# Optimization experiments

Hardware: AMD Instinct MI355X
Metric: run time of the kernel (lower is better)

## Reference

```python
import jax, jax.numpy as jnp
import numpy as np

B, T, C, H = 4096, 96, 256, 64  # batch, seq (<= BLOCK_SIZE=96), N_EMBED, head_size


def setup_inputs() -> dict:
    key = jax.random.key(0)
    k1, k2, k3, k4 = jax.random.split(key, 4)
    x = jax.random.normal(k1, (B, T, C), dtype=jnp.float32)
    # nn.Linear(C, H, bias=False) stores W as [H, C]; we keep [C, H] so y = x @ W.
    scale = 1.0 / jnp.sqrt(C)
    Wk = jax.random.normal(k2, (C, H), dtype=jnp.float32) * scale
    Wq = jax.random.normal(k3, (C, H), dtype=jnp.float32) * scale
    Wv = jax.random.normal(k4, (C, H), dtype=jnp.float32) * scale
    return {"x": x, "Wk": Wk, "Wq": Wq, "Wv": Wv}


def reference(x, Wk, Wq, Wv):
    Bx, Tx, Cx = x.shape
    k = x @ Wk                      # [B, T, H]
    q = x @ Wq                      # [B, T, H]
    v = x @ Wv                      # [B, T, H]
    # NOTE: original scales by C**-0.5 (embed dim), not head_size**-0.5.
    wei = jnp.einsum('bth,bsh->bts', q, k) * (Cx ** -0.5)  # [B, T, T]
    causal = jnp.tril(jnp.ones((Tx, Tx), dtype=bool))
    wei = jnp.where(causal, wei, -jnp.inf)
    wei = jax.nn.softmax(wei, axis=-1)
    # dropout is identity at eval time
    return jnp.einsum('bts,bsh->bth', wei, v)  # [B, T, H]
```

## Files before the change

kernel.cpp:

```cpp
#include <hip/hip_runtime.h>
#include <cstddef>


typedef __bf16 bf16x8 __attribute__((ext_vector_type(8)));
typedef float f32x4 __attribute__((ext_vector_type(4)));

#define GLOAD_LDS16(gp, lp)                                                     \
  __builtin_amdgcn_global_load_lds(                                             \
      (const __attribute__((address_space(1))) void*)(gp),                      \
      (__attribute__((address_space(3))) void*)(lp), 16, 0, 0)

static __device__ __forceinline__ unsigned short f2bf_u16(float f) {
  union { float f; unsigned int u; } c; c.f = f;
  return (unsigned short)((c.u + 0x7FFFu + ((c.u >> 16) & 1u)) >> 16);
}

__global__ void pack_w(const float* __restrict__ Wk, const float* __restrict__ Wq,
                       const float* __restrict__ Wv, unsigned short* __restrict__ pack) {
  int idx = blockIdx.x * blockDim.x + threadIdx.x;
  if (idx >= 6144) return;
  int lane = idx & 63;
  int t = idx >> 6;
  int nt = t & 3;
  int p  = (t >> 2) % 3;
  int kt = t / 12;
  const float* W = (p == 0) ? Wk : (p == 1) ? Wq : Wv;
  int k0 = kt * 32 + (lane >> 4) * 8;
  int n  = nt * 16 + (lane & 15);
  unsigned short* dst = pack + (size_t)idx * 8;
#pragma unroll
  for (int j = 0; j < 8; ++j) dst[j] = f2bf_u16(W[(size_t)(k0 + j) * 64 + n]);
}

#define LDK 72
#define LDP 104
#define LDV 104

__global__ __launch_bounds__(768, 6) void head_fused(
    const float* __restrict__ x, const unsigned short* __restrict__ pack,
    float* __restrict__ out) {
  __shared__ __attribute__((aligned(16))) unsigned char smem[68352];
  unsigned short* SA  = (unsigned short*)smem;
  unsigned short* ks2 = (unsigned short*)(smem + 39936);
  float*          rsm = (float*)(smem + 67584);

  const int w    = threadIdx.x >> 6;
  const int half = w >= 6;
  const int w6   = w - 6 * half;
  const int lane = threadIdx.x & 63;
  const int lo   = lane & 15;
  const int hi   = lane >> 4;

  const int bb = 2 * blockIdx.x + half;
  const float* __restrict__ xb = x + (size_t)bb * (96 * 256);

  unsigned short* SAh  = SA  + half * (96 * LDP);
  unsigned short* ks2h = ks2 + half * (96 * LDK);
  float*          rsh  = rsm + half * 96;

  f32x4 acc[3][4];
#pragma unroll
  for (int p = 0; p < 3; ++p)
#pragma unroll
    for (int nt = 0; nt < 4; ++nt) acc[p][nt] = (f32x4){0.f, 0.f, 0.f, 0.f};

  const int am = 16 * w6 + lo;
  const float* xrow = xb + (size_t)am * 256 + hi * 8;

  GLOAD_LDS16((const char*)pack + (size_t)threadIdx.x * 16,
              smem + (size_t)w * 1024);
  f32x4 a0 = *(const f32x4*)(xrow);
  f32x4 a1 = *(const f32x4*)(xrow + 4);
  __syncthreads();

  for (int kt = 0; kt < 8; ++kt) {
    const int cur = kt & 1;
    f32x4 na0, na1;
    if (kt < 7) {
      GLOAD_LDS16((const char*)pack + (size_t)(kt + 1) * 12288 + (size_t)threadIdx.x * 16,
                  smem + (size_t)(1 - cur) * 12288 + (size_t)w * 1024);
      na0 = *(const f32x4*)(xrow + (kt + 1) * 32);
      na1 = *(const f32x4*)(xrow + (kt + 1) * 32 + 4);
    }
    union { bf16x8 v; unsigned short u[8]; } af;
#pragma unroll
    for (int j = 0; j < 4; ++j) { af.u[j] = f2bf_u16(a0[j]); af.u[4 + j] = f2bf_u16(a1[j]); }
    const unsigned short* pb = (const unsigned short*)(smem + cur * 12288);
#pragma unroll
    for (int p = 0; p < 3; ++p) {
#pragma unroll
      for (int nt = 0; nt < 4; ++nt) {
        bf16x8 bf = *(const bf16x8*)(pb + ((p * 4 + nt) * 64 + lane) * 8);
        acc[p][nt] = __builtin_amdgcn_mfma_f32_16x16x32_bf16(af.v, bf, acc[p][nt], 0, 0, 0);
      }
    }
    if (kt < 7) { a0 = na0; a1 = na1; }
    __syncthreads();
  }

  unsigned short vv[16];
#pragma unroll
  for (int nt = 0; nt < 4; ++nt) {
#pragma unroll
    for (int r = 0; r < 4; ++r) {
      int row = 16 * w6 + hi * 4 + r;
      int col = 16 * nt + lo;
      ks2h[row * LDK + col] = f2bf_u16(acc[0][nt][r]);
      SAh [row * LDP + col] = f2bf_u16(acc[1][nt][r]);
      vv[nt * 4 + r] = f2bf_u16(acc[2][nt][r]);
    }
  }
  __syncthreads();

  f32x4 sacc[6];
#pragma unroll
  for (int jt = 0; jt < 6; ++jt) sacc[jt] = (f32x4){0.f, 0.f, 0.f, 0.f};

  bf16x8 qf0 = *(const bf16x8*)(SAh + (16 * w6 + lo) * LDP + hi * 8);
  bf16x8 qf1 = *(const bf16x8*)(SAh + (16 * w6 + lo) * LDP + 32 + hi * 8);
  for (int jt = 0; jt <= w6; ++jt) {
    bf16x8 kf0 = *(const bf16x8*)(ks2h + (16 * jt + lo) * LDK + hi * 8);
    bf16x8 kf1 = *(const bf16x8*)(ks2h + (16 * jt + lo) * LDK + 32 + hi * 8);
    sacc[jt] = __builtin_amdgcn_mfma_f32_16x16x32_bf16(qf0, kf0, sacc[jt], 0, 0, 0);
    sacc[jt] = __builtin_amdgcn_mfma_f32_16x16x32_bf16(qf1, kf1, sacc[jt], 0, 0, 0);
  }

#pragma unroll
  for (int r = 0; r < 4; ++r) {
    int row = 16 * w6 + hi * 4 + r;
    float pr[6];
    float mx = -1e30f;
    for (int jt = 0; jt <= w6; ++jt) {
      int col = 16 * jt + lo;
      float s = sacc[jt][r] * 0.0625f;
      s = (col <= row) ? s : -1e30f;
      pr[jt] = s;
      mx = fmaxf(mx, s);
    }
#pragma unroll
    for (int off = 1; off < 16; off <<= 1) mx = fmaxf(mx, __shfl_xor(mx, off, 64));
    float sum = 0.f;
    for (int jt = 0; jt <= w6; ++jt) {
      float p = __expf(pr[jt] - mx);
      pr[jt] = p;
      sum += p;
    }
#pragma unroll
    for (int off = 1; off < 16; off <<= 1) sum += __shfl_xor(sum, off, 64);
#pragma unroll
    for (int jt = 0; jt < 6; ++jt) {
      float p = (jt <= w6) ? pr[jt] : 0.f;
      SAh[row * LDP + 16 * jt + lo] = f2bf_u16(p);
    }
    if (lo == 0) rsh[row] = sum;
  }
  __syncthreads();

  unsigned short* vT = ks2h;
#pragma unroll
  for (int nt = 0; nt < 4; ++nt) {
#pragma unroll
    for (int r = 0; r < 4; ++r) {
      int row = 16 * w6 + hi * 4 + r;
      int col = 16 * nt + lo;
      vT[col * LDV + row] = vv[nt * 4 + r];
    }
  }
  __syncthreads();

  f32x4 oacc[4];
#pragma unroll
  for (int nt = 0; nt < 4; ++nt) oacc[nt] = (f32x4){0.f, 0.f, 0.f, 0.f};

  const int ksmax = (16 * w6 + 15) >> 5;
  for (int ks = 0; ks <= ksmax; ++ks) {
    bf16x8 pf = *(const bf16x8*)(SAh + (16 * w6 + lo) * LDP + ks * 32 + hi * 8);
#pragma unroll
    for (int nt = 0; nt < 4; ++nt) {
      bf16x8 vf = *(const bf16x8*)(vT + (16 * nt + lo) * LDV + ks * 32 + hi * 8);
      oacc[nt] = __builtin_amdgcn_mfma_f32_16x16x32_bf16(pf, vf, oacc[nt], 0, 0, 0);
    }
  }

  float* __restrict__ ob = out + (size_t)bb * (96 * 64);
#pragma unroll
  for (int r = 0; r < 4; ++r) {
    int row = 16 * w6 + hi * 4 + r;
    float inv = 1.0f / rsh[row];
#pragma unroll
    for (int nt = 0; nt < 4; ++nt) {
      ob[row * 64 + 16 * nt + lo] = oacc[nt][r] * inv;
    }
  }
}

extern "C" void kernel_launch(void* const* d_in, const int* in_sizes, int n_in,
                              void* d_out, int out_size, void* d_ws, size_t ws_size,
                              hipStream_t stream) {
  const float* x  = (const float*)d_in[0];
  const float* Wk = (const float*)d_in[1];
  const float* Wq = (const float*)d_in[2];
  const float* Wv = (const float*)d_in[3];
  float* out = (float*)d_out;
  unsigned short* pack = (unsigned short*)d_ws;

  const int B = in_sizes[0] / (96 * 256);

  pack_w<<<24, 256, 0, stream>>>(Wk, Wq, Wv, pack);
  head_fused<<<B / 2, 768, 0, stream>>>(x, pack, out);
}
```

Before: 662.1 us.

## Deepen QKV projection pipeline and stage output through LDS for coalesced stores

The QKV projection loop is restructured to process two k-tiles per barrier. Packed weights for two k-steps are loaded into double-buffered 24 KB LDS regions, and x rows are prefetched two iterations ahead in registers. Explicit s_waitcnt vmcnt and raw s_barrier calls replace __syncthreads. The aim is to keep more global loads in flight and halve the number of barriers in the memory-latency-bound projection. The epilogue now writes normalized outputs to LDS and stores them back as 16-byte vectors, which makes the global writes coalesced. The cost is extra register pressure and one more block-wide barrier.

```diff
diff --git a/kernel.cpp b/kernel.cpp
--- a/kernel.cpp
+++ b/kernel.cpp
@@ -9,6 +9,10 @@
   __builtin_amdgcn_global_load_lds(                                             \
       (const __attribute__((address_space(1))) void*)(gp),                      \
       (__attribute__((address_space(3))) void*)(lp), 16, 0, 0)
+
+#define FENCE() asm volatile("" ::: "memory")
+#define WAITVM(N) asm volatile("s_waitcnt vmcnt(" #N ")" ::: "memory")
+#define BAR() do { __builtin_amdgcn_s_barrier(); FENCE(); } while (0)
 
 static __device__ __forceinline__ unsigned short f2bf_u16(float f) {
   union { float f; unsigned int u; } c; c.f = f;
@@ -67,34 +71,86 @@
   const int am = 16 * w6 + lo;
   const float* xrow = xb + (size_t)am * 256 + hi * 8;
 
-  GLOAD_LDS16((const char*)pack + (size_t)threadIdx.x * 16,
-              smem + (size_t)w * 1024);
-  f32x4 a0 = *(const f32x4*)(xrow);
-  f32x4 a1 = *(const f32x4*)(xrow + 4);
-  __syncthreads();
-
-  for (int kt = 0; kt < 8; ++kt) {
-    const int cur = kt & 1;
-    f32x4 na0, na1;
-    if (kt < 7) {
-      GLOAD_LDS16((const char*)pack + (size_t)(kt + 1) * 12288 + (size_t)threadIdx.x * 16,
-                  smem + (size_t)(1 - cur) * 12288 + (size_t)w * 1024);
-      na0 = *(const f32x4*)(xrow + (kt + 1) * 32);
-      na1 = *(const f32x4*)(xrow + (kt + 1) * 32 + 4);
-    }
-    union { bf16x8 v; unsigned short u[8]; } af;
-#pragma unroll
-    for (int j = 0; j < 4; ++j) { af.u[j] = f2bf_u16(a0[j]); af.u[4 + j] = f2bf_u16(a1[j]); }
-    const unsigned short* pb = (const unsigned short*)(smem + cur * 12288);
-#pragma unroll
-    for (int p = 0; p < 3; ++p) {
+  f32x4 A0[4], A1[4];
+
+#define XLOAD(SL, IT) do {                         \
+    const float* xp_ = xrow + (IT) * 64;           \
+    SL[0] = *(const f32x4*)(xp_);                  \
+    SL[1] = *(const f32x4*)(xp_ + 4);              \
+    SL[2] = *(const f32x4*)(xp_ + 32);             \
+    SL[3] = *(const f32x4*)(xp_ + 36);             \
+  } while (0)
+
+#define STAGE(IT, BUFOFS) do {                                                        \
+    const char* g_ = (const char*)pack + (size_t)(2 * (IT)) * 12288                   \
+                     + (size_t)threadIdx.x * 16;                                      \
+    GLOAD_LDS16(g_,         smem + (BUFOFS) + (size_t)w * 1024);                      \
+    GLOAD_LDS16(g_ + 12288, smem + (BUFOFS) + 12288 + (size_t)w * 1024);              \
+    FENCE();                                                                          \
+  } while (0)
+
+  union bfu { bf16x8 v; unsigned short u[8]; };
+
+  auto conv = [&](const f32x4* SL, bfu& af0_, bfu& af1_) {
+#pragma unroll
+    for (int j = 0; j < 4; ++j) {
+      af0_.u[j]     = f2bf_u16(SL[0][j]);
+      af0_.u[4 + j] = f2bf_u16(SL[1][j]);
+      af1_.u[j]     = f2bf_u16(SL[2][j]);
+      af1_.u[4 + j] = f2bf_u16(SL[3][j]);
+    }
+  };
+  auto mfma24 = [&](int bufofs, bf16x8 af0_, bf16x8 af1_) {
+    const unsigned short* pb = (const unsigned short*)(smem + bufofs);
+#pragma unroll
+    for (int p = 0; p < 3; ++p)
 #pragma unroll
       for (int nt = 0; nt < 4; ++nt) {
-        bf16x8 bf = *(const bf16x8*)(pb + ((p * 4 + nt) * 64 + lane) * 8);
-        acc[p][nt] = __builtin_amdgcn_mfma_f32_16x16x32_bf16(af.v, bf, acc[p][nt], 0, 0, 0);
+        bf16x8 b0 = *(const bf16x8*)(pb + ((p * 4 + nt) * 64 + lane) * 8);
+        acc[p][nt] = __builtin_amdgcn_mfma_f32_16x16x32_bf16(af0_, b0, acc[p][nt], 0, 0, 0);
       }
-    }
-    if (kt < 7) { a0 = na0; a1 = na1; }
+    const unsigned short* pb1 = pb + 6144;
+#pragma unroll
+    for (int p = 0; p < 3; ++p)
+#pragma unroll
+      for (int nt = 0; nt < 4; ++nt) {
+        bf16x8 b1 = *(const bf16x8*)(pb1 + ((p * 4 + nt) * 64 + lane) * 8);
+        acc[p][nt] = __builtin_amdgcn_mfma_f32_16x16x32_bf16(af1_, b1, acc[p][nt], 0, 0, 0);
+      }
+  };
+
+  STAGE(0, 0);
+  XLOAD(A0, 0);
+  XLOAD(A1, 1);
+  WAITVM(8);
+  BAR();
+
+  {
+    STAGE(1, 24576);
+    bfu af0_, af1_; conv(A0, af0_, af1_);
+    XLOAD(A0, 2);
+    mfma24(0, af0_.v, af1_.v);
+    WAITVM(4);
+    BAR();
+  }
+  {
+    STAGE(2, 0);
+    bfu af0_, af1_; conv(A1, af0_, af1_);
+    XLOAD(A1, 3);
+    mfma24(24576, af0_.v, af1_.v);
+    WAITVM(4);
+    BAR();
+  }
+  {
+    STAGE(3, 24576);
+    bfu af0_, af1_; conv(A0, af0_, af1_);
+    mfma24(0, af0_.v, af1_.v);
+    WAITVM(0);
+    BAR();
+  }
+  {
+    bfu af0_, af1_; conv(A1, af0_, af1_);
+    mfma24(24576, af0_.v, af1_.v);
     __syncthreads();
   }
 
@@ -182,15 +238,20 @@
     }
   }
 
+  __syncthreads();
+  float* ot = (float*)(smem + (size_t)w * 4096);
+#pragma unroll
+  for (int r = 0; r < 4; ++r) {
+    float inv = 1.0f / rsh[16 * w6 + hi * 4 + r];
+#pragma unroll
+    for (int nt = 0; nt < 4; ++nt)
+      ot[(hi * 4 + r) * 64 + 16 * nt + lo] = oacc[nt][r] * inv;
+  }
   float* __restrict__ ob = out + (size_t)bb * (96 * 64);
 #pragma unroll
-  for (int r = 0; r < 4; ++r) {
-    int row = 16 * w6 + hi * 4 + r;
-    float inv = 1.0f / rsh[row];
-#pragma unroll
-    for (int nt = 0; nt < 4; ++nt) {
-      ob[row * 64 + 16 * nt + lo] = oacc[nt][r] * inv;
-    }
+  for (int i = 0; i < 4; ++i) {
+    f32x4 o4 = *(const f32x4*)(ot + (i * 4 + hi) * 64 + lo * 4);
+    *(f32x4*)(ob + (size_t)(16 * w6 + i * 4 + hi) * 64 + lo * 4) = o4;
   }
 }
 
```

After: 734.5 us. 1.11x slower.

## Use explicit vmcnt waits and barriers in projection loop; stage output via LDS

Applied to the files above, without the earlier changes.

The projection K-loop replaces __syncthreads with a manual s_waitcnt vmcnt(2) plus s_barrier, so the next x-row register prefetch stays in flight while the LDS weight tile is waited on. The last iteration is peeled out of the loop. The QK and softmax loops are fully unrolled over a fixed 6 tiles, with predication instead of runtime trip counts. The output is staged through per-wave LDS and written as coalesced 16-byte stores instead of scattered scalar stores. These changes add one extra barrier and depend on hand-placed waitcnt counts matching the number of outstanding loads.

```diff
diff --git a/kernel.cpp b/kernel.cpp
--- a/kernel.cpp
+++ b/kernel.cpp
@@ -9,6 +9,10 @@
   __builtin_amdgcn_global_load_lds(                                             \
       (const __attribute__((address_space(1))) void*)(gp),                      \
       (__attribute__((address_space(3))) void*)(lp), 16, 0, 0)
+
+#define FENCE() asm volatile("" ::: "memory")
+#define WAITVM(N) asm volatile("s_waitcnt vmcnt(" #N ")" ::: "memory")
+#define BAR() do { __builtin_amdgcn_s_barrier(); FENCE(); } while (0)
 
 static __device__ __forceinline__ unsigned short f2bf_u16(float f) {
   union { float f; unsigned int u; } c; c.f = f;
@@ -69,32 +73,47 @@
 
   GLOAD_LDS16((const char*)pack + (size_t)threadIdx.x * 16,
               smem + (size_t)w * 1024);
+  FENCE();
   f32x4 a0 = *(const f32x4*)(xrow);
   f32x4 a1 = *(const f32x4*)(xrow + 4);
-  __syncthreads();
-
-  for (int kt = 0; kt < 8; ++kt) {
+  WAITVM(2);
+  BAR();
+
+  for (int kt = 0; kt < 7; ++kt) {
     const int cur = kt & 1;
-    f32x4 na0, na1;
-    if (kt < 7) {
-      GLOAD_LDS16((const char*)pack + (size_t)(kt + 1) * 12288 + (size_t)threadIdx.x * 16,
-                  smem + (size_t)(1 - cur) * 12288 + (size_t)w * 1024);
-      na0 = *(const f32x4*)(xrow + (kt + 1) * 32);
-      na1 = *(const f32x4*)(xrow + (kt + 1) * 32 + 4);
-    }
+    GLOAD_LDS16((const char*)pack + (size_t)(kt + 1) * 12288 + (size_t)threadIdx.x * 16,
+                smem + (size_t)(1 - cur) * 12288 + (size_t)w * 1024);
+    FENCE();
+    f32x4 na0 = *(const f32x4*)(xrow + (kt + 1) * 32);
+    f32x4 na1 = *(const f32x4*)(xrow + (kt + 1) * 32 + 4);
+
     union { bf16x8 v; unsigned short u[8]; } af;
 #pragma unroll
     for (int j = 0; j < 4; ++j) { af.u[j] = f2bf_u16(a0[j]); af.u[4 + j] = f2bf_u16(a1[j]); }
     const unsigned short* pb = (const unsigned short*)(smem + cur * 12288);
 #pragma unroll
-    for (int p = 0; p < 3; ++p) {
+    for (int p = 0; p < 3; ++p)
 #pragma unroll
       for (int nt = 0; nt < 4; ++nt) {
         bf16x8 bf = *(const bf16x8*)(pb + ((p * 4 + nt) * 64 + lane) * 8);
         acc[p][nt] = __builtin_amdgcn_mfma_f32_16x16x32_bf16(af.v, bf, acc[p][nt], 0, 0, 0);
       }
-    }
-    if (kt < 7) { a0 = na0; a1 = na1; }
+    a0 = na0; a1 = na1;
+    WAITVM(2);
+    BAR();
+  }
+  {
+    union { bf16x8 v; unsigned short u[8]; } af;
+#pragma unroll
+    for (int j = 0; j < 4; ++j) { af.u[j] = f2bf_u16(a0[j]); af.u[4 + j] = f2bf_u16(a1[j]); }
+    const unsigned short* pb = (const unsigned short*)(smem + 12288);
+#pragma unroll
+    for (int p = 0; p < 3; ++p)
+#pragma unroll
+      for (int nt = 0; nt < 4; ++nt) {
+        bf16x8 bf = *(const bf16x8*)(pb + ((p * 4 + nt) * 64 + lane) * 8);
+        acc[p][nt] = __builtin_amdgcn_mfma_f32_16x16x32_bf16(af.v, bf, acc[p][nt], 0, 0, 0);
+      }
     __syncthreads();
   }
 
@@ -118,11 +137,14 @@
 
   bf16x8 qf0 = *(const bf16x8*)(SAh + (16 * w6 + lo) * LDP + hi * 8);
   bf16x8 qf1 = *(const bf16x8*)(SAh + (16 * w6 + lo) * LDP + 32 + hi * 8);
-  for (int jt = 0; jt <= w6; ++jt) {
-    bf16x8 kf0 = *(const bf16x8*)(ks2h + (16 * jt + lo) * LDK + hi * 8);
-    bf16x8 kf1 = *(const bf16x8*)(ks2h + (16 * jt + lo) * LDK + 32 + hi * 8);
-    sacc[jt] = __builtin_amdgcn_mfma_f32_16x16x32_bf16(qf0, kf0, sacc[jt], 0, 0, 0);
-    sacc[jt] = __builtin_amdgcn_mfma_f32_16x16x32_bf16(qf1, kf1, sacc[jt], 0, 0, 0);
+#pragma unroll
+  for (int jt = 0; jt < 6; ++jt) {
+    if (jt <= w6) {
+      bf16x8 kf0 = *(const bf16x8*)(ks2h + (16 * jt + lo) * LDK + hi * 8);
+      bf16x8 kf1 = *(const bf16x8*)(ks2h + (16 * jt + lo) * LDK + 32 + hi * 8);
+      sacc[jt] = __builtin_amdgcn_mfma_f32_16x16x32_bf16(qf0, kf0, sacc[jt], 0, 0, 0);
+      sacc[jt] = __builtin_amdgcn_mfma_f32_16x16x32_bf16(qf1, kf1, sacc[jt], 0, 0, 0);
+    }
   }
 
 #pragma unroll
@@ -130,7 +152,8 @@
     int row = 16 * w6 + hi * 4 + r;
     float pr[6];
     float mx = -1e30f;
-    for (int jt = 0; jt <= w6; ++jt) {
+#pragma unroll
+    for (int jt = 0; jt < 6; ++jt) {
       int col = 16 * jt + lo;
       float s = sacc[jt][r] * 0.0625f;
       s = (col <= row) ? s : -1e30f;
@@ -140,7 +163,8 @@
 #pragma unroll
     for (int off = 1; off < 16; off <<= 1) mx = fmaxf(mx, __shfl_xor(mx, off, 64));
     float sum = 0.f;
-    for (int jt = 0; jt <= w6; ++jt) {
+#pragma unroll
+    for (int jt = 0; jt < 6; ++jt) {
       float p = __expf(pr[jt] - mx);
       pr[jt] = p;
       sum += p;
@@ -148,10 +172,8 @@
 #pragma unroll
     for (int off = 1; off < 16; off <<= 1) sum += __shfl_xor(sum, off, 64);
 #pragma unroll
-    for (int jt = 0; jt < 6; ++jt) {
-      float p = (jt <= w6) ? pr[jt] : 0.f;
-      SAh[row * LDP + 16 * jt + lo] = f2bf_u16(p);
-    }
+    for (int jt = 0; jt < 6; ++jt)
+      SAh[row * LDP + 16 * jt + lo] = f2bf_u16(pr[jt]);
     if (lo == 0) rsh[row] = sum;
   }
   __syncthreads();
@@ -182,15 +204,20 @@
     }
   }
 
+  __syncthreads();
+  float* ot = (float*)(smem + (size_t)w * 4096);
+#pragma unroll
+  for (int r = 0; r < 4; ++r) {
+    float inv = 1.0f / rsh[16 * w6 + hi * 4 + r];
+#pragma unroll
+    for (int nt = 0; nt < 4; ++nt)
+      ot[(hi * 4 + r) * 64 + 16 * nt + lo] = oacc[nt][r] * inv;
+  }
   float* __restrict__ ob = out + (size_t)bb * (96 * 64);
 #pragma unroll
-  for (int r = 0; r < 4; ++r) {
-    int row = 16 * w6 + hi * 4 + r;
-    float inv = 1.0f / rsh[row];
-#pragma unroll
-    for (int nt = 0; nt < 4; ++nt) {
-      ob[row * 64 + 16 * nt + lo] = oacc[nt][r] * inv;
-    }
+  for (int i = 0; i < 4; ++i) {
+    f32x4 o4 = *(const f32x4*)(ot + (i * 4 + hi) * 64 + lo * 4);
+    *(f32x4*)(ob + (size_t)(16 * w6 + i * 4 + hi) * 64 + lo * 4) = o4;
   }
 }
 
```

Measured after the change: 567.9 us. -14.2%, faster.
